# Kernel tuning notes

Hardware: AMD Instinct MI355X
Metric: run time of the kernel (lower is better)

The kernel has to match this reference:

```python
import jax, jax.numpy as jnp
import numpy as np

B, C, H, W = 16, 256, 32, 32
DIM = H * W  # LayerNorm/Linear dim == h*w per the rearrange in forward


def _conv1x1(x, w, b):
    # x: [b,c,h,w], w: [out,in] (1x1 kernel squeezed), b: [out]
    return jnp.einsum('bchw,oc->bohw', x, w) + b[None, :, None, None]


def _layernorm(x, g, b, eps=1e-5):
    mu = jnp.mean(x, axis=-1, keepdims=True)
    var = jnp.var(x, axis=-1, keepdims=True)
    return (x - mu) / jnp.sqrt(var + eps) * g + b


def setup_inputs() -> dict:
    key = jax.random.key(0)
    ks = jax.random.split(key, 12)
    n = jax.random.normal
    k_cdc = (2.0 / (2 * C)) ** 0.5   # kaiming_normal fan_in = 2C
    k_v = (2.0 / C) ** 0.5           # fan_in = C
    k_lin = (2.0 / DIM) ** 0.5       # fan_in = DIM
    return {
        'x_spa': n(ks[0], (B, C, H, W), jnp.float32),
        'x_freq': n(ks[1], (B, C, H, W), jnp.float32),
        'w_cdc': n(ks[2], (C, 2 * C), jnp.float32) * k_cdc,
        'b_cdc': jnp.zeros((C,), jnp.float32),
        'w_sv': n(ks[3], (C, C), jnp.float32) * k_v,
        'b_sv': jnp.zeros((C,), jnp.float32),
        'w_fv': n(ks[4], (C, C), jnp.float32) * k_v,
        'b_fv': jnp.zeros((C,), jnp.float32),
        'ln_w': jnp.ones((DIM,), jnp.float32),
        'ln_b': jnp.zeros((DIM,), jnp.float32),
        'w_qk': n(ks[5], (2 * DIM, DIM), jnp.float32) * k_lin,  # Linear(dim, 2*dim), no bias
        'w_spa': n(ks[6], (DIM, DIM), jnp.float32) * k_lin,
        'b_spa': jnp.zeros((DIM,), jnp.float32),
        'w_frq': n(ks[7], (DIM, DIM), jnp.float32) * k_lin,
        'b_frq': jnp.zeros((DIM,), jnp.float32),
    }


def reference(x_spa, x_freq, w_cdc, b_cdc, w_sv, b_sv, w_fv, b_fv,
              ln_w, ln_b, w_qk, w_spa, b_spa, w_frq, b_frq):
    b, c, h, w = x_spa.shape
    hw = h * w
    scale = hw ** (-0.5)
    v_spa = _conv1x1(x_spa, w_sv, b_sv).reshape(b, c, hw)
    v_freq = _conv1x1(x_freq, w_fv, b_fv).reshape(b, c, hw)
    x = _conv1x1(jnp.concatenate([x_spa, x_freq], axis=1), w_cdc, b_cdc).reshape(b, c, hw)
    x = _layernorm(x, ln_w, ln_b)
    qk = x @ w_qk.T                       # [b, c, 2*hw]
    q, k = jnp.split(qk, 2, axis=-1)      # each [b, c, hw]
    att = jnp.einsum('bcn,bcm->bnm', q, k) * scale   # q^T k over channels: [b, hw, hw]
    att_spa = jax.nn.softmax(att @ w_spa.T + b_spa, axis=-1)
    att_frq = jax.nn.softmax(att @ w_frq.T + b_frq, axis=-1)
    out_spa = x_spa + jnp.einsum('bcn,bnm->bcm', v_spa, att_spa).reshape(b, c, h, w)
    out_freq = x_freq + jnp.einsum('bcn,bnm->bcm', v_freq, att_frq).reshape(b, c, h, w)
    return out_spa, out_freq
```

## Files before the change

### kernel.cpp

```cpp
#include <hip/hip_runtime.h>
#include <hip/hip_bf16.h>

typedef __hip_bfloat16 bf16;
typedef __attribute__((ext_vector_type(8))) short bf16x8v;
typedef __attribute__((ext_vector_type(4))) float f32x4v;

__device__ __forceinline__ float bfbits2f(unsigned short h) {
    union { unsigned int u; float f; } v; v.u = ((unsigned int)h) << 16; return v.f;
}
__device__ __forceinline__ unsigned short f2bfbits(float f) {
    bf16 h = __float2bfloat16(f);
    unsigned short s;
    __builtin_memcpy(&s, &h, 2);
    return s;
}
__device__ __forceinline__ float load1_any(const void* p, long idx, bool f32) {
    if (f32) return ((const float*)p)[idx];
    return bfbits2f(((const unsigned short*)p)[idx]);
}
__device__ __forceinline__ float4 loadbf4(const bf16* p) {
    ushort4 u = *reinterpret_cast<const ushort4*>(p);
    return make_float4(bfbits2f(u.x), bfbits2f(u.y), bfbits2f(u.z), bfbits2f(u.w));
}
__device__ __forceinline__ void store_bf4(bf16* p, float a, float b, float c, float d) {
    ushort4 o;
    o.x = f2bfbits(a); o.y = f2bfbits(b); o.z = f2bfbits(c); o.w = f2bfbits(d);
    *reinterpret_cast<ushort4*>(p) = o;
}
__device__ __forceinline__ void gl16(const void* g, void* l) {
    __builtin_amdgcn_global_load_lds(
        (const __attribute__((address_space(1))) unsigned int*)g,
        (__attribute__((address_space(3))) unsigned int*)l, 16, 0, 0);
}

__global__ __launch_bounds__(1024)
void detect_kernel(const unsigned short* __restrict__ x, int* __restrict__ flag) {
    const int tid = threadIdx.x;
    int zc = 0, hc = 0;
    const uint4* xv = (const uint4*)x;
#pragma unroll
    for (int p = 0; p < 16; ++p) {
        uint4 v = xv[p * 1024 + tid];
        unsigned s0 = v.x & 0xFFFFu, s1 = v.y & 0xFFFFu;
        unsigned s2 = v.z & 0xFFFFu, s3 = v.w & 0xFFFFu;
        zc += (int)(s0 == 0) + (int)(s1 == 0) + (int)(s2 == 0) + (int)(s3 == 0);
        hc += (int)(((s0 >> 7) & 0xFFu) >= 0x90u) + (int)(((s1 >> 7) & 0xFFu) >= 0x90u)
            + (int)(((s2 >> 7) & 0xFFu) >= 0x90u) + (int)(((s3 >> 7) & 0xFFu) >= 0x90u);
    }
#pragma unroll
    for (int off = 32; off > 0; off >>= 1) {
        zc += __shfl_down(zc, off);
        hc += __shfl_down(hc, off);
    }
    __shared__ int rz[16], rh[16];
    if ((tid & 63) == 0) { rz[tid >> 6] = zc; rh[tid >> 6] = hc; }
    __syncthreads();
    if (tid == 0) {
        int Z = 0, H = 0;
#pragma unroll
        for (int i = 0; i < 16; ++i) { Z += rz[i]; H += rh[i]; }
        flag[0] = (Z > 60000 || H > 256) ? 1 : 0;
        flag[1] = 1;
    }
}

__global__ void diag_kernel(float* __restrict__ out, float val) {
    if (threadIdx.x == 0) out[0] = val;
}

__global__ __launch_bounds__(256)
void convert6_kernel(const void* __restrict__ s0, const void* __restrict__ s1,
                     const void* __restrict__ s2, const void* __restrict__ s3,
                     const void* __restrict__ s4, const void* __restrict__ s5,
                     bf16* __restrict__ dst, const int* __restrict__ dflag) {
    const bool f32 = (*dflag != 0);
    for (long i = (long)blockIdx.x * 256 + threadIdx.x; i < 4456448;
         i += (long)gridDim.x * 256) {
        const void* s; long o;
        if (i < 131072)       { s = s0; o = i; }
        else if (i < 196608)  { s = s1; o = i - 131072; }
        else if (i < 262144)  { s = s2; o = i - 196608; }
        else if (i < 2359296) { s = s3; o = i - 262144; }
        else if (i < 3407872) { s = s4; o = i - 2359296; }
        else                  { s = s5; o = i - 3407872; }
        dst[i] = __float2bfloat16(load1_any(s, o, f32));
    }
}

__global__ __launch_bounds__(256)
void xpose_w_kernel(const bf16* __restrict__ src, bf16* __restrict__ dst) {
    __shared__ float t[64][65];
    const int c0 = blockIdx.x * 64, r0 = blockIdx.y * 64;
    const int tid = threadIdx.x;
#pragma unroll
    for (int p = 0; p < 16; ++p) {
        int e = tid + p * 256; int r = e >> 6, c = e & 63;
        t[r][c] = __bfloat162float(src[(long)(r0 + r) * 1024 + c0 + c]);
    }
    __syncthreads();
#pragma unroll
    for (int p = 0; p < 16; ++p) {
        int e = tid + p * 256; int r = e >> 6, c = e & 63;
        dst[(long)(c0 + r) * 1024 + r0 + c] = __float2bfloat16(t[c][r]);
    }
}

__global__ __launch_bounds__(256)
void build_wleft_kernel(const bf16* __restrict__ w_cdc, const bf16* __restrict__ w_sv,
                        const bf16* __restrict__ w_fv, bf16* __restrict__ W) {
    int i = blockIdx.x * 256 + threadIdx.x;
    if (i >= 393216) return;
    int r = i >> 9, c = i & 511;
    float v = 0.f;
    if (r < 256) v = __bfloat162float(w_cdc[r * 512 + c]);
    else if (r < 512) { if (c < 256) v = __bfloat162float(w_sv[(r - 256) * 256 + c]); }
    else              { if (c >= 256) v = __bfloat162float(w_fv[(r - 512) * 256 + (c - 256)]); }
    W[i] = __float2bfloat16(v);
}

__global__ __launch_bounds__(256)
void build_bcat_kernel(const void* __restrict__ b0, const void* __restrict__ b1,
                       const void* __restrict__ b2, float* __restrict__ bc,
                       const int* __restrict__ dflag) {
    const bool f32 = (*dflag != 0);
    int i = blockIdx.x * 256 + threadIdx.x;
    if (i < 256)      bc[i] = load1_any(b0, i, f32);
    else if (i < 512) bc[i] = load1_any(b1, i - 256, f32);
    else if (i < 768) bc[i] = load1_any(b2, i - 512, f32);
}

__global__ __launch_bounds__(256)
void xpose_conv_kernel(const void* __restrict__ x1, const void* __restrict__ x2,
                       bf16* __restrict__ dst, int bofs, int zsplit,
                       const int* __restrict__ dflag) {
    const bool f32 = (*dflag != 0);
    __shared__ float t[64][65];
    const int ch0 = blockIdx.y * 64, n0 = blockIdx.x * 64, z = blockIdx.z;
    const bool hiz = (z >= zsplit);
    const int zl = hiz ? z - zsplit : z;
    const void* x = hiz ? x2 : x1;
    const long sb = (long)(zl + bofs) * 262144, db = (long)z * 262144;
    const int tid = threadIdx.x;
#pragma unroll
    for (int p = 0; p < 16; ++p) {
        int e = tid + p * 256; int sch = e >> 6, sn = e & 63;
        t[sch][sn] = load1_any(x, sb + (long)(ch0 + sch) * 1024 + n0 + sn, f32);
    }
    __syncthreads();
#pragma unroll
    for (int p = 0; p < 16; ++p) {
        int e = tid + p * 256; int dn = e >> 6, dch = e & 63;
        dst[db + (long)(n0 + dn) * 256 + ch0 + dch] = __float2bfloat16(t[dch][dn]);
    }
}

__global__ __launch_bounds__(256)
void smnorm_kernel(bf16* __restrict__ X, bf16* __restrict__ vb, int gN, int gq) {
    const int tid = threadIdx.x;
    const int cg = tid & 7;
    const int js = tid >> 3;
    const int n0 = blockIdx.x * 64;
    const long zb = (long)blockIdx.y * 1048576;
    unsigned short* Xp = (unsigned short*)X + zb + n0 + cg * 8;

    float m[8];
#pragma unroll
    for (int q = 0; q < 8; ++q) m[q] = -3.4e38f;
#pragma unroll 4
    for (int r = 0; r < 32; ++r) {
        bf16x8v u = *(const bf16x8v*)(Xp + (long)(js * 32 + r) * 1024);
#pragma unroll
        for (int q = 0; q < 8; ++q)
            m[q] = fmaxf(m[q], bfbits2f((unsigned short)u[q]));
    }
    __shared__ float sh[32][8][8];
    __shared__ float Mc[64];
    __shared__ float Sc[64];
#pragma unroll
    for (int q = 0; q < 8; ++q) sh[js][cg][q] = m[q];
    __syncthreads();
    if (tid < 64) {
        float mm = -3.4e38f;
#pragma unroll 8
        for (int s = 0; s < 32; ++s) mm = fmaxf(mm, sh[s][tid >> 3][tid & 7]);
        Mc[tid] = mm;
    }
    __syncthreads();
    float M8[8], s8[8];
#pragma unroll
    for (int q = 0; q < 8; ++q) { M8[q] = Mc[cg * 8 + q]; s8[q] = 0.f; }
#pragma unroll 4
    for (int r = 0; r < 32; ++r) {
        long off = (long)(js * 32 + r) * 1024;
        bf16x8v u = *(const bf16x8v*)(Xp + off);
        bf16x8v o;
#pragma unroll
        for (int q = 0; q < 8; ++q) {
            float e = __expf(bfbits2f((unsigned short)u[q]) - M8[q]);
            s8[q] += e;
            o[q] = (short)f2bfbits(e);
        }
        *(bf16x8v*)(Xp + off) = o;
    }
    __syncthreads();
#pragma unroll
    for (int q = 0; q < 8; ++q) sh[js][cg][q] = s8[q];
    __syncthreads();
    if (tid < 64) {
        float ss = 0.f;
#pragma unroll 8
        for (int s = 0; s < 32; ++s) ss += sh[s][tid >> 3][tid & 7];
        Sc[tid] = 1.0f / ss;
    }
    __syncthreads();
    const int side = (blockIdx.y >= (unsigned)gq) ? 1 : 0;
    const int zl = blockIdx.y - side * gq;
    bf16* vp = vb + (long)(side * 256) * gN + (long)zl * 1024 + n0 + cg * 8;
    float is8[8];
#pragma unroll
    for (int q = 0; q < 8; ++q) is8[q] = Sc[cg * 8 + q];
#pragma unroll
    for (int rr = 0; rr < 8; ++rr) {
        long off = (long)(rr * 32 + js) * gN;
        bf16x8v u = *(bf16x8v*)(vp + off);
        bf16x8v o;
#pragma unroll
        for (int q = 0; q < 8; ++q)
            o[q] = (short)f2bfbits(bfbits2f((unsigned short)u[q]) * is8[q]);
        *(bf16x8v*)(vp + off) = o;
    }
}

template <int MI, int EPI>
__global__ __launch_bounds__(256)
void mfma_nt(const bf16* __restrict__ A1, const bf16* __restrict__ A2,
             long aB1, long aB2, int ldA1, int ldA2,
             const bf16* __restrict__ B1, const bf16* __restrict__ B2,
             long bB1, long bB2, int ldB1, int ldB2,
             int ksplit, long kOff2,
             void* __restrict__ out1, void* __restrict__ out2,
             long oB1, long oB2, int ldO1, int ldO2,
             int K, float scale,
             const void* __restrict__ bias1, const void* __restrict__ bias2,
             const void* __restrict__ res1, const void* __restrict__ res2,
             long rBatch, int bofs, int zsplit,
             const int* __restrict__ dflag) {
    constexpr int BM = MI * 32;
    __shared__ short As[3][BM * 32];
    __shared__ short Bs[3][4096];
    const int tid  = threadIdx.x;
    const int lane = tid & 63, wave = tid >> 6;
    const int quad = lane >> 4, lrow = lane & 15;
    const int wm = (wave >> 1) * (MI * 16), wn = (wave & 1) * 64;

    int bx = blockIdx.x, by = blockIdx.y, bz = blockIdx.z;
    {
        const int gx = gridDim.x, gy = gridDim.y;
        const int gxy = gx * gy;
        const int ntot = gxy * gridDim.z;
        if ((ntot & 7) == 0) {
            int flat = bx + gx * (by + gy * bz);
            int w = (flat & 7) * (ntot >> 3) + (flat >> 3);
            bz = w / gxy;
            int rem = w - bz * gxy;
            by = rem / gx;
            bx = rem - by * gx;
        }
    }
    const int z  = bz;
    const bool hiz = (z >= zsplit);
    const int zl = hiz ? z - zsplit : z;
    const int n0 = bx * 128, m0 = by * BM;
    const int ldA = hiz ? ldA2 : ldA1, ldB = hiz ? ldB2 : ldB1;
    const int ldO = hiz ? ldO2 : ldO1;
    const int srow = tid >> 2, sseg = tid & 3;
    const int sl = sseg ^ ((srow >> 1) & 3);
    const int xq = quad ^ ((lrow >> 1) & 3);

    const bf16* Ab = (hiz ? A2 : A1) + (long)zl * (hiz ? aB2 : aB1);
    const bf16* Bb = (hiz ? B2 : B1) + (long)zl * (hiz ? bB2 : bB1);

    auto stage = [&](int buf, int k0) {
        const bf16* asrc = Ab + (long)k0;
        const bf16* bsrc = Bb + ((k0 < ksplit) ? (long)k0 : (long)(k0 - ksplit) + kOff2);
#pragma unroll
        for (int p = 0; p < MI / 2; ++p)
            gl16(asrc + (long)(m0 + p * 64 + srow) * ldA + sl * 8,
                 &As[buf][p * 2048 + wave * 512]);
        gl16(bsrc + (long)(n0 + srow) * ldB + sl * 8, &Bs[buf][wave * 512]);
        gl16(bsrc + (long)(n0 + 64 + srow) * ldB + sl * 8, &Bs[buf][2048 + wave * 512]);
    };

    f32x4v acc[MI][4] = {};
    const int nt = K >> 5;
    stage(0, 0);
    if (nt > 1) stage(1, 32);

    int cur = 0;
    for (int t = 0; t < nt; ++t) {
        if (t + 1 < nt) {
            if constexpr (MI == 4) asm volatile("s_waitcnt vmcnt(4)" ::: "memory");
            else                   asm volatile("s_waitcnt vmcnt(3)" ::: "memory");
        } else {
            asm volatile("s_waitcnt vmcnt(0)" ::: "memory");
        }
        __builtin_amdgcn_s_barrier();
        __builtin_amdgcn_sched_barrier(0);
        if (t + 2 < nt) {
            int nb = cur + 2; if (nb >= 3) nb -= 3;
            stage(nb, (t + 2) << 5);
        }
        bf16x8v bfr[4], afr[MI];
#pragma unroll
        for (int j = 0; j < 4; ++j)
            bfr[j] = *(const bf16x8v*)&Bs[cur][(wn + j * 16 + lrow) * 32 + xq * 8];
#pragma unroll
        for (int i = 0; i < MI; ++i)
            afr[i] = *(const bf16x8v*)&As[cur][(wm + i * 16 + lrow) * 32 + xq * 8];
        __builtin_amdgcn_s_setprio(1);
#pragma unroll
        for (int i = 0; i < MI; ++i)
#pragma unroll
            for (int j = 0; j < 4; ++j)
                acc[i][j] = __builtin_amdgcn_mfma_f32_16x16x32_bf16(afr[i], bfr[j], acc[i][j], 0, 0, 0);
        __builtin_amdgcn_s_setprio(0);
        cur = (cur == 2) ? 0 : cur + 1;
    }

    const bool f32 = (*dflag != 0);
    const void* bias = hiz ? bias2 : bias1;
    if (EPI != 3) {
        bf16* O = (bf16*)(hiz ? out2 : out1) + (long)zl * (hiz ? oB2 : oB1);
#pragma unroll
        for (int i = 0; i < MI; ++i) {
            int row0 = m0 + wm + i * 16 + quad * 4;
            float rb[4] = {0.f, 0.f, 0.f, 0.f};
            if (EPI == 1 || EPI == 2) {
#pragma unroll
                for (int r = 0; r < 4; ++r) rb[r] = load1_any(bias, row0 + r, f32);
            }
#pragma unroll
            for (int j = 0; j < 4; ++j) {
                int col = n0 + wn + j * 16 + lrow;
#pragma unroll
                for (int r = 0; r < 4; ++r) {
                    float vv = acc[i][j][r];
                    if (EPI == 1) vv += rb[r];
                    if (EPI == 2) vv = vv * scale + rb[r];
                    O[(long)(row0 + r) * ldO + col] = __float2bfloat16(vv);
                }
            }
        }
    } else {
        float* O = (float*)(hiz ? out2 : out1);
        const void* res = hiz ? res2 : res1;
        const long ob  = (long)(zl + bofs) * (hiz ? oB2 : oB1);
        const long rbb = (long)(zl + bofs) * rBatch;
#pragma unroll
        for (int i = 0; i < MI; ++i) {
            int row0 = m0 + wm + i * 16 + quad * 4;
#pragma unroll
            for (int j = 0; j < 4; ++j) {
                int col = n0 + wn + j * 16 + lrow;
#pragma unroll
                for (int r = 0; r < 4; ++r) {
                    float rv = load1_any(res, rbb + (long)(row0 + r) * ldO + col, f32);
                    O[ob + (long)(row0 + r) * ldO + col] = acc[i][j][r] + rv;
                }
            }
        }
    }
}

__global__ __launch_bounds__(256)
void layernorm_kernel(const bf16* __restrict__ src, bf16* __restrict__ dst,
                      const void* __restrict__ g, const void* __restrict__ beta,
                      int gN, const int* __restrict__ dflag) {
    const bool f32 = (*dflag != 0);
    const int zc = blockIdx.x;
    const int zz = zc >> 8, c = zc & 255;
    const bf16* p = src + (long)c * gN + (long)zz * 1024;
    bf16* q = dst + (long)zc * 1024;
    const int tid = threadIdx.x;
    float4 v = loadbf4(p + tid * 4);
    float s  = v.x + v.y + v.z + v.w;
    float ss = v.x * v.x + v.y * v.y + v.z * v.z + v.w * v.w;
#pragma unroll
    for (int off = 32; off > 0; off >>= 1) {
        s  += __shfl_down(s, off);
        ss += __shfl_down(ss, off);
    }
    __shared__ float sh[8];
    __shared__ float sh_mu, sh_rs;
    if ((tid & 63) == 0) { sh[tid >> 6] = s; sh[4 + (tid >> 6)] = ss; }
    __syncthreads();
    if (tid == 0) {
        float S  = sh[0] + sh[1] + sh[2] + sh[3];
        float SS = sh[4] + sh[5] + sh[6] + sh[7];
        float mu = S * (1.0f / 1024.0f);
        float var = SS * (1.0f / 1024.0f) - mu * mu;
        sh_mu = mu;
        sh_rs = rsqrtf(fmaxf(var, 0.0f) + 1e-5f);
    }
    __syncthreads();
    float mu = sh_mu, rs = sh_rs;
    float gx = load1_any(g, tid * 4 + 0, f32), gy = load1_any(g, tid * 4 + 1, f32);
    float gz = load1_any(g, tid * 4 + 2, f32), gw = load1_any(g, tid * 4 + 3, f32);
    float bx = load1_any(beta, tid * 4 + 0, f32), by = load1_any(beta, tid * 4 + 1, f32);
    float bz = load1_any(beta, tid * 4 + 2, f32), bw = load1_any(beta, tid * 4 + 3, f32);
    store_bf4(q + tid * 4,
              (v.x - mu) * rs * gx + bx, (v.y - mu) * rs * gy + by,
              (v.z - mu) * rs * gz + bz, (v.w - mu) * rs * gw + bw);
}

extern "C" void kernel_launch(void* const* d_in, const int* in_sizes, int n_in,
                              void* d_out, int out_size, void* d_ws, size_t ws_size,
                              hipStream_t stream) {
    const void* x_spa  = d_in[0];
    const void* x_freq = d_in[1];
    const void* w_cdc  = d_in[2];
    const void* b_cdc  = d_in[3];
    const void* w_sv   = d_in[4];
    const void* b_sv   = d_in[5];
    const void* w_fv   = d_in[6];
    const void* b_fv   = d_in[7];
    const void* ln_w   = d_in[8];
    const void* ln_b   = d_in[9];
    const void* w_qk   = d_in[10];
    const void* w_spa  = d_in[11];
    const void* b_spa  = d_in[12];
    const void* w_frq  = d_in[13];
    const void* b_frq  = d_in[14];
    float* out = (float*)d_out;

    const int B = 16, C = 256;
    const long XB = 262144;
    const long PB = 1048576;

    int*   dflag = (int*)d_ws;
    float* bcat  = (float*)((char*)d_ws + 1024);
    bf16*  wb    = (bf16*)((char*)d_ws + 4096);
    bf16* w_cdc_b = wb;
    bf16* w_sv_b  = w_cdc_b + 131072;
    bf16* w_fv_b  = w_sv_b  + 65536;
    bf16* w_qk_b  = w_fv_b  + 65536;
    bf16* w_spa_b = w_qk_b  + 2097152;
    bf16* w_frq_b = w_spa_b + 1048576;
    bf16* w_qk_hiT= w_frq_b + 1048576;
    bf16* W1f     = w_qk_hiT + 1048576;
    bf16* Wleft   = W1f + 1048576;
    bf16* pb      = Wleft + 393216;

    const size_t fixedB = 4096 + 6946816ull * 2;
    const size_t perB   = 8921088ull;
    size_t avail = (ws_size > fixedB) ? (ws_size - fixedB) : 0;
    long gmax = (long)(avail / perB);
    const bool wsOK = (gmax >= 1);
    int G = wsOK ? (int)(gmax > 16 ? 16 : gmax) : 1;

    bf16* xT    = pb;
    bf16* XV    = xT  + 2L * G * XB;
    bf16* xln2  = XV  + 3L * G * XB;
    bf16* qTT   = xln2 + (long)G * XB;
    bf16* attpT = qTT + 3L * G * XB;

    dim3 blk(256);
    detect_kernel<<<dim3(1), dim3(1024), 0, stream>>>((const unsigned short*)x_spa, dflag);

    if (!wsOK) {
        float mb = (float)(ws_size >> 20);
        diag_kernel<<<dim3(1), dim3(64), 0, stream>>>(out, 1000.0f * (mb + 1.0f));
        return;
    }

    convert6_kernel<<<dim3(4352), blk, 0, stream>>>(w_cdc, w_sv, w_fv, w_qk, w_spa, w_frq,
                                                    wb, dflag);
    xpose_w_kernel<<<dim3(16, 16), blk, 0, stream>>>(w_qk_b + 1048576, w_qk_hiT);
    build_wleft_kernel<<<dim3(1536), blk, 0, stream>>>(w_cdc_b, w_sv_b, w_fv_b, Wleft);
    build_bcat_kernel<<<dim3(3), blk, 0, stream>>>(b_cdc, b_sv, b_fv, bcat, dflag);
    mfma_nt<4, 0><<<dim3(8, 8, 2), blk, 0, stream>>>(
        w_spa_b, w_frq_b, 0, 0, 1024, 1024,
        w_qk_hiT, w_qk_hiT, 0, 0, 1024, 1024, 1024, 0,
        w_qk_b + 1048576, W1f, 0, 0, 1024, 1024,
        1024, 1.0f, nullptr, nullptr, nullptr, nullptr, 0, 0, 1, dflag);

    for (int b0 = 0; b0 < B; b0 += G) {
        int g = (B - b0 < G) ? (B - b0) : G;
        const int gN = g * 1024;
        bf16* vb = XV + 256L * gN;

        xpose_conv_kernel<<<dim3(16, 4, 2 * g), blk, 0, stream>>>(
            x_spa, x_freq, xT, b0, g, dflag);

        mfma_nt<4, 1><<<dim3(8 * g, 6, 1), blk, 0, stream>>>(
            Wleft, Wleft, 0, 0, 512, 512,
            xT, xT, 0, 0, 256, 256, 256, (long)g * XB,
            XV, XV, 0, 0, gN, gN,
            512, 1.0f, bcat, bcat, nullptr, nullptr, 0, 0, 1, dflag + 1);

        layernorm_kernel<<<dim3(g * C), blk, 0, stream>>>(XV, xln2, ln_w, ln_b, gN, dflag);

        mfma_nt<4, 0><<<dim3(2 * g, 8, 3), blk, 0, stream>>>(
            w_qk_b, W1f, 1048576, 0, 1024, 1024,
            xln2, xln2, 0, 0, 1024, 1024, 1024, 0,
            qTT, qTT + 2L * g * XB, (long)g * XB, 0, g * 256, g * 256,
            1024, 1.0f, nullptr, nullptr, nullptr, nullptr, 0, 0, 2, dflag);

        mfma_nt<4, 2><<<dim3(8, 8, 2 * g), blk, 0, stream>>>(
            qTT + (long)g * XB, qTT + 2L * g * XB, 256, 256, g * 256, g * 256,
            qTT, qTT, 256, 256, g * 256, g * 256, 256, 0,
            attpT, attpT + (long)g * PB, PB, PB, 1024, 1024,
            256, 0.03125f, b_spa, b_frq, nullptr, nullptr, 0, 0, g, dflag);

        smnorm_kernel<<<dim3(16, 2 * g), blk, 0, stream>>>(attpT, vb, gN, g);

        mfma_nt<4, 3><<<dim3(8, 2, 2 * g), blk, 0, stream>>>(
            vb, vb + 256L * gN, 1024, 1024, gN, gN,
            attpT, attpT + (long)g * PB, PB, PB, 1024, 1024, 1024, 0,
            out, out + 4194304, XB, XB, 1024, 1024,
            1024, 1.0f, nullptr, nullptr, x_spa, x_freq, XB, b0, g, dflag);
    }
}
```

Measured before the change: 349.2 us.

## Deepen GEMM LDS pipeline to five stages and fold weight prep kernels

Adds a template parameter for the number of shared-memory buffers in the MFMA GEMM. Most GEMMs now prefetch four K-tiles ahead, with vmcnt waits set to match, to hide more global load latency. The cost is more LDS per block and possibly lower occupancy. The setprio calls around the MFMA loop are removed. The Wleft and bias-concatenation builder kernels are merged into convert6_kernel, which reads the raw inputs directly and saves two launches.

```diff
diff --git a/kernel.cpp b/kernel.cpp
--- a/kernel.cpp
+++ b/kernel.cpp
@@ -72,18 +72,37 @@
 void convert6_kernel(const void* __restrict__ s0, const void* __restrict__ s1,
                      const void* __restrict__ s2, const void* __restrict__ s3,
                      const void* __restrict__ s4, const void* __restrict__ s5,
-                     bf16* __restrict__ dst, const int* __restrict__ dflag) {
+                     const void* __restrict__ b0, const void* __restrict__ b1,
+                     const void* __restrict__ b2,
+                     bf16* __restrict__ dst, bf16* __restrict__ wl,
+                     float* __restrict__ bc, const int* __restrict__ dflag) {
     const bool f32 = (*dflag != 0);
-    for (long i = (long)blockIdx.x * 256 + threadIdx.x; i < 4456448;
+    for (long i = (long)blockIdx.x * 256 + threadIdx.x; i < 4850432;
          i += (long)gridDim.x * 256) {
-        const void* s; long o;
-        if (i < 131072)       { s = s0; o = i; }
-        else if (i < 196608)  { s = s1; o = i - 131072; }
-        else if (i < 262144)  { s = s2; o = i - 196608; }
-        else if (i < 2359296) { s = s3; o = i - 262144; }
-        else if (i < 3407872) { s = s4; o = i - 2359296; }
-        else                  { s = s5; o = i - 3407872; }
-        dst[i] = __float2bfloat16(load1_any(s, o, f32));
+        if (i < 4456448) {
+            const void* s; long o;
+            if (i < 131072)       { s = s0; o = i; }
+            else if (i < 196608)  { s = s1; o = i - 131072; }
+            else if (i < 262144)  { s = s2; o = i - 196608; }
+            else if (i < 2359296) { s = s3; o = i - 262144; }
+            else if (i < 3407872) { s = s4; o = i - 2359296; }
+            else                  { s = s5; o = i - 3407872; }
+            dst[i] = __float2bfloat16(load1_any(s, o, f32));
+        } else if (i < 4849664) {
+            long j = i - 4456448;
+            int r = (int)(j >> 9), c = (int)(j & 511);
+            float v = 0.f;
+            if (r < 256) v = load1_any(s0, r * 512 + c, f32);
+            else if (r < 512) { if (c < 256) v = load1_any(s1, (r - 256) * 256 + c, f32); }
+            else              { if (c >= 256) v = load1_any(s2, (r - 512) * 256 + (c - 256), f32); }
+            wl[j] = __float2bfloat16(v);
+        } else {
+            long j = i - 4849664;
+            float v = (j < 256) ? load1_any(b0, j, f32)
+                    : (j < 512) ? load1_any(b1, j - 256, f32)
+                                : load1_any(b2, j - 512, f32);
+            bc[j] = v;
+        }
     }
 }
 
@@ -103,30 +122,6 @@
         int e = tid + p * 256; int r = e >> 6, c = e & 63;
         dst[(long)(c0 + r) * 1024 + r0 + c] = __float2bfloat16(t[c][r]);
     }
-}
-
-__global__ __launch_bounds__(256)
-void build_wleft_kernel(const bf16* __restrict__ w_cdc, const bf16* __restrict__ w_sv,
-                        const bf16* __restrict__ w_fv, bf16* __restrict__ W) {
-    int i = blockIdx.x * 256 + threadIdx.x;
-    if (i >= 393216) return;
-    int r = i >> 9, c = i & 511;
-    float v = 0.f;
-    if (r < 256) v = __bfloat162float(w_cdc[r * 512 + c]);
-    else if (r < 512) { if (c < 256) v = __bfloat162float(w_sv[(r - 256) * 256 + c]); }
-    else              { if (c >= 256) v = __bfloat162float(w_fv[(r - 512) * 256 + (c - 256)]); }
-    W[i] = __float2bfloat16(v);
-}
-
-__global__ __launch_bounds__(256)
-void build_bcat_kernel(const void* __restrict__ b0, const void* __restrict__ b1,
-                       const void* __restrict__ b2, float* __restrict__ bc,
-                       const int* __restrict__ dflag) {
-    const bool f32 = (*dflag != 0);
-    int i = blockIdx.x * 256 + threadIdx.x;
-    if (i < 256)      bc[i] = load1_any(b0, i, f32);
-    else if (i < 512) bc[i] = load1_any(b1, i - 256, f32);
-    else if (i < 768) bc[i] = load1_any(b2, i - 512, f32);
 }
 
 __global__ __launch_bounds__(256)
@@ -231,7 +226,7 @@
     }
 }
 
-template <int MI, int EPI>
+template <int MI, int EPI, int NBUF>
 __global__ __launch_bounds__(256)
 void mfma_nt(const bf16* __restrict__ A1, const bf16* __restrict__ A2,
              long aB1, long aB2, int ldA1, int ldA2,
@@ -246,8 +241,9 @@
              long rBatch, int bofs, int zsplit,
              const int* __restrict__ dflag) {
     constexpr int BM = MI * 32;
-    __shared__ short As[3][BM * 32];
-    __shared__ short Bs[3][4096];
+    constexpr int LPS = MI / 2 + 2;
+    __shared__ short As[NBUF][BM * 32];
+    __shared__ short Bs[NBUF][4096];
     const int tid  = threadIdx.x;
     const int lane = tid & 63, wave = tid >> 6;
     const int quad = lane >> 4, lrow = lane & 15;
@@ -295,20 +291,39 @@
     const int nt = K >> 5;
     stage(0, 0);
     if (nt > 1) stage(1, 32);
+    if constexpr (NBUF >= 5) {
+        if (nt > 2) stage(2, 64);
+        if (nt > 3) stage(3, 96);
+    }
 
     int cur = 0;
     for (int t = 0; t < nt; ++t) {
-        if (t + 1 < nt) {
-            if constexpr (MI == 4) asm volatile("s_waitcnt vmcnt(4)" ::: "memory");
-            else                   asm volatile("s_waitcnt vmcnt(3)" ::: "memory");
+        const int rem = nt - 1 - t;
+        if constexpr (NBUF == 3) {
+            if (rem >= 1) {
+                if constexpr (LPS == 4) asm volatile("s_waitcnt vmcnt(4)" ::: "memory");
+                else                    asm volatile("s_waitcnt vmcnt(3)" ::: "memory");
+            } else {
+                asm volatile("s_waitcnt vmcnt(0)" ::: "memory");
+            }
         } else {
-            asm volatile("s_waitcnt vmcnt(0)" ::: "memory");
+            if constexpr (LPS == 4) {
+                if (rem >= 3)      asm volatile("s_waitcnt vmcnt(12)" ::: "memory");
+                else if (rem == 2) asm volatile("s_waitcnt vmcnt(8)" ::: "memory");
+                else if (rem == 1) asm volatile("s_waitcnt vmcnt(4)" ::: "memory");
+                else               asm volatile("s_waitcnt vmcnt(0)" ::: "memory");
+            } else {
+                if (rem >= 3)      asm volatile("s_waitcnt vmcnt(9)" ::: "memory");
+                else if (rem == 2) asm volatile("s_waitcnt vmcnt(6)" ::: "memory");
+                else if (rem == 1) asm volatile("s_waitcnt vmcnt(3)" ::: "memory");
+                else               asm volatile("s_waitcnt vmcnt(0)" ::: "memory");
+            }
         }
         __builtin_amdgcn_s_barrier();
         __builtin_amdgcn_sched_barrier(0);
-        if (t + 2 < nt) {
-            int nb = cur + 2; if (nb >= 3) nb -= 3;
-            stage(nb, (t + 2) << 5);
+        if (t + NBUF - 1 < nt) {
+            int nb = cur + NBUF - 1; if (nb >= NBUF) nb -= NBUF;
+            stage(nb, (t + NBUF - 1) << 5);
         }
         bf16x8v bfr[4], afr[MI];
 #pragma unroll
@@ -317,14 +332,12 @@
 #pragma unroll
         for (int i = 0; i < MI; ++i)
             afr[i] = *(const bf16x8v*)&As[cur][(wm + i * 16 + lrow) * 32 + xq * 8];
-        __builtin_amdgcn_s_setprio(1);
 #pragma unroll
         for (int i = 0; i < MI; ++i)
 #pragma unroll
             for (int j = 0; j < 4; ++j)
                 acc[i][j] = __builtin_amdgcn_mfma_f32_16x16x32_bf16(afr[i], bfr[j], acc[i][j], 0, 0, 0);
-        __builtin_amdgcn_s_setprio(0);
-        cur = (cur == 2) ? 0 : cur + 1;
+        cur = (cur + 1 == NBUF) ? 0 : cur + 1;
     }
 
     const bool f32 = (*dflag != 0);
@@ -473,12 +486,11 @@
         return;
     }
 
-    convert6_kernel<<<dim3(4352), blk, 0, stream>>>(w_cdc, w_sv, w_fv, w_qk, w_spa, w_frq,
-                                                    wb, dflag);
+    convert6_kernel<<<dim3(4352), blk, 0, stream>>>(
+        w_cdc, w_sv, w_fv, w_qk, w_spa, w_frq, b_cdc, b_sv, b_fv,
+        wb, Wleft, bcat, dflag);
     xpose_w_kernel<<<dim3(16, 16), blk, 0, stream>>>(w_qk_b + 1048576, w_qk_hiT);
-    build_wleft_kernel<<<dim3(1536), blk, 0, stream>>>(w_cdc_b, w_sv_b, w_fv_b, Wleft);
-    build_bcat_kernel<<<dim3(3), blk, 0, stream>>>(b_cdc, b_sv, b_fv, bcat, dflag);
-    mfma_nt<4, 0><<<dim3(8, 8, 2), blk, 0, stream>>>(
+    mfma_nt<4, 0, 5><<<dim3(8, 8, 2), blk, 0, stream>>>(
         w_spa_b, w_frq_b, 0, 0, 1024, 1024,
         w_qk_hiT, w_qk_hiT, 0, 0, 1024, 1024, 1024, 0,
         w_qk_b + 1048576, W1f, 0, 0, 1024, 1024,
@@ -492,7 +504,7 @@
         xpose_conv_kernel<<<dim3(16, 4, 2 * g), blk, 0, stream>>>(
             x_spa, x_freq, xT, b0, g, dflag);
 
-        mfma_nt<4, 1><<<dim3(8 * g, 6, 1), blk, 0, stream>>>(
+        mfma_nt<4, 1, 5><<<dim3(8 * g, 6, 1), blk, 0, stream>>>(
             Wleft, Wleft, 0, 0, 512, 512,
             xT, xT, 0, 0, 256, 256, 256, (long)g * XB,
             XV, XV, 0, 0, gN, gN,
@@ -500,13 +512,13 @@
 
         layernorm_kernel<<<dim3(g * C), blk, 0, stream>>>(XV, xln2, ln_w, ln_b, gN, dflag);
 
-        mfma_nt<4, 0><<<dim3(2 * g, 8, 3), blk, 0, stream>>>(
+        mfma_nt<4, 0, 5><<<dim3(2 * g, 8, 3), blk, 0, stream>>>(
             w_qk_b, W1f, 1048576, 0, 1024, 1024,
             xln2, xln2, 0, 0, 1024, 1024, 1024, 0,
             qTT, qTT + 2L * g * XB, (long)g * XB, 0, g * 256, g * 256,
             1024, 1.0f, nullptr, nullptr, nullptr, nullptr, 0, 0, 2, dflag);
 
-        mfma_nt<4, 2><<<dim3(8, 8, 2 * g), blk, 0, stream>>>(
+        mfma_nt<4, 2, 3><<<dim3(8, 8, 2 * g), blk, 0, stream>>>(
             qTT + (long)g * XB, qTT + 2L * g * XB, 256, 256, g * 256, g * 256,
             qTT, qTT, 256, 256, g * 256, g * 256, 256, 0,
             attpT, attpT + (long)g * PB, PB, PB, 1024, 1024,
@@ -514,7 +526,7 @@
 
         smnorm_kernel<<<dim3(16, 2 * g), blk, 0, stream>>>(attpT, vb, gN, g);
 
-        mfma_nt<4, 3><<<dim3(8, 2, 2 * g), blk, 0, stream>>>(
+        mfma_nt<4, 3, 5><<<dim3(8, 2, 2 * g), blk, 0, stream>>>(
             vb, vb + 256L * gN, 1024, 1024, gN, gN,
             attpT, attpT + (long)g * PB, PB, PB, 1024, 1024, 1024, 0,
             out, out + 4194304, XB, XB, 1024, 1024,
```

New measurement: 368.4 us. +5.5%, slower.
